# Optimization experiments

Hardware: AMD Instinct MI355X
Metric: run time of the kernel (lower is better)

Reference implementation:

```python
import jax, jax.numpy as jnp
from jax import lax
import numpy as np

H = 64  # hiddenSize
I = 9   # inputSize

def _init_lstm_params(key, in_dim, hidden):
    k = 1.0 / np.sqrt(hidden)
    ks = jax.random.split(key, 4)
    w_ih = jax.random.uniform(ks[0], (4 * hidden, in_dim), minval=-k, maxval=k, dtype=jnp.float32)
    w_hh = jax.random.uniform(ks[1], (4 * hidden, hidden), minval=-k, maxval=k, dtype=jnp.float32)
    b_ih = jax.random.uniform(ks[2], (4 * hidden,), minval=-k, maxval=k, dtype=jnp.float32)
    b_hh = jax.random.uniform(ks[3], (4 * hidden,), minval=-k, maxval=k, dtype=jnp.float32)
    return w_ih, w_hh, b_ih, b_hh

def setup_inputs() -> dict:
    key = jax.random.key(0)
    kx, k0, k1, kl = jax.random.split(key, 4)
    x = jax.random.normal(kx, (4096, 336, I), dtype=jnp.float32)
    w_ih0, w_hh0, b_ih0, b_hh0 = _init_lstm_params(k0, I, H)
    w_ih1, w_hh1, b_ih1, b_hh1 = _init_lstm_params(k1, H, H)
    klw, klb = jax.random.split(kl)
    k = 1.0 / np.sqrt(H)
    w_lin = jax.random.uniform(klw, (1, H), minval=-k, maxval=k, dtype=jnp.float32)
    b_lin = jax.random.uniform(klb, (1,), minval=-k, maxval=k, dtype=jnp.float32)
    return {"x": x, "w_ih0": w_ih0, "w_hh0": w_hh0, "b_ih0": b_ih0, "b_hh0": b_hh0,
            "w_ih1": w_ih1, "w_hh1": w_hh1, "b_ih1": b_ih1, "b_hh1": b_hh1,
            "w_lin": w_lin, "b_lin": b_lin}

def _lstm_layer(x_seq, w_ih, w_hh, b_ih, b_hh):
    # x_seq: [B, T, D] -> hidden sequence [B, T, H]. PyTorch gate order: i, f, g, o.
    B = x_seq.shape[0]
    hidden = w_hh.shape[1]
    # Precompute input contribution for all timesteps in one GEMM.
    pre = jnp.einsum('btd,gd->btg', x_seq, w_ih) + b_ih + b_hh  # [B, T, 4H]
    pre_t = jnp.swapaxes(pre, 0, 1)  # [T, B, 4H]

    def step(carry, p):
        h, c = carry
        gates = p + h @ w_hh.T  # [B, 4H]
        i, f, g, o = jnp.split(gates, 4, axis=-1)
        i = jax.nn.sigmoid(i)
        f = jax.nn.sigmoid(f)
        g = jnp.tanh(g)
        o = jax.nn.sigmoid(o)
        c = f * c + i * g
        h = o * jnp.tanh(c)
        return (h, c), h

    h0 = jnp.zeros((B, hidden), dtype=x_seq.dtype)
    c0 = jnp.zeros((B, hidden), dtype=x_seq.dtype)
    _, hs = lax.scan(step, (h0, c0), pre_t)
    return jnp.swapaxes(hs, 0, 1)  # [B, T, H]

def reference(x, w_ih0, w_hh0, b_ih0, b_hh0, w_ih1, w_hh1, b_ih1, b_hh1, w_lin, b_lin):
    h1 = _lstm_layer(x, w_ih0, w_hh0, b_ih0, b_hh0)     # layer 1 (dropout inactive in eval)
    h2 = _lstm_layer(h1, w_ih1, w_hh1, b_ih1, b_hh1)    # layer 2
    last = h2[:, -1, :]                                  # [B, H]
    out = jax.nn.sigmoid(last @ w_lin.T + b_lin)         # [B, 1]
    return out
```

## Files before the change

### kernel.cpp

```cpp
#include <hip/hip_runtime.h>
#include <hip/hip_bf16.h>
#include <stdint.h>


typedef __attribute__((ext_vector_type(8))) short s16x8;
typedef __attribute__((ext_vector_type(4))) short s16x4;
typedef __attribute__((ext_vector_type(4))) float f32x4;

#define MFMA_BF16 __builtin_amdgcn_mfma_f32_16x16x32_bf16
#define LOG2E     1.4426950408889634f
#define TWO_LOG2E 2.8853900817779268f

__device__ __forceinline__ short f2bf(float f) {
    uint32_t u = __builtin_bit_cast(uint32_t, f);
    u += 0x7fffu + ((u >> 16) & 1u);
    return (short)(u >> 16);
}

__device__ __forceinline__ s16x4 pack_bf16x4(float a, float b, float c, float d) {
    union { uint32_t u[2]; s16x4 s; } r;
    asm("v_cvt_pk_bf16_f32 %0, %1, %2" : "=v"(r.u[0]) : "v"(a), "v"(b));
    asm("v_cvt_pk_bf16_f32 %0, %1, %2" : "=v"(r.u[1]) : "v"(c), "v"(d));
    return r.s;
}

static __device__ __forceinline__ float fexp2(float t){ return __builtin_amdgcn_exp2f(t); }
static __device__ __forceinline__ float frcp (float t){ return __builtin_amdgcn_rcpf(t); }

__device__ __forceinline__ float rcp1p2(float t) {
    return frcp(1.0f + fexp2(t));
}

__device__ __forceinline__ f32x4 nonlin_wide(const f32x4 acc[4], f32x4& cs) {
    float e0[4], e1[4], e2[4], e3[4];
    #pragma unroll
    for (int r = 0; r < 4; ++r) {
        e0[r] = fexp2(acc[0][r]);
        e1[r] = fexp2(acc[1][r]);
        e2[r] = fexp2(acc[2][r]);
        e3[r] = fexp2(acc[3][r]);
    }
    float iv[4], fv[4], gq[4], ov[4];
    #pragma unroll
    for (int r = 0; r < 4; ++r) {
        iv[r] = frcp(1.f + e0[r]);
        fv[r] = frcp(1.f + e1[r]);
        gq[r] = frcp(1.f + e2[r]);
        ov[r] = frcp(1.f + e3[r]);
    }
    float ec[4];
    #pragma unroll
    for (int r = 0; r < 4; ++r) {
        float gvs = fmaf(-2.f * TWO_LOG2E, gq[r], TWO_LOG2E);
        cs[r] = fmaf(fv[r], cs[r], iv[r] * gvs);
        ec[r] = fexp2(cs[r]);
    }
    f32x4 h;
    #pragma unroll
    for (int r = 0; r < 4; ++r) {
        float th = fmaf(-2.f, frcp(1.f + ec[r]), 1.f);
        h[r] = ov[r] * th;
    }
    return h;
}

__global__ __launch_bounds__(512, 1)
void lstm_fused(const float* __restrict__ x,
                const float* __restrict__ w_ih0, const float* __restrict__ w_hh0,
                const float* __restrict__ b_ih0, const float* __restrict__ b_hh0,
                const float* __restrict__ w_ih1, const float* __restrict__ w_hh1,
                const float* __restrict__ b_ih1, const float* __restrict__ b_hh1,
                const float* __restrict__ w_lin, const float* __restrict__ b_lin,
                float* __restrict__ out)
{
    __shared__ __align__(16) short xs[16 * 512];
    __shared__ __align__(16) short h0s[2][16 * 64];
    __shared__ __align__(16) short h1s[16 * 64];
    __shared__ float red[4][16];

    const int tid  = threadIdx.x;
    const int w    = tid >> 6;
    const int role = w >> 2;
    const int wl   = w & 3;
    const int l    = tid & 63;
    const int bcol = l & 15;
    const int q    = l >> 4;
    const int b0   = blockIdx.x * 16;

    for (int i = tid; i < 16 * 512; i += 512) xs[i] = 0;
    for (int i = tid; i < 16 * 64; i += 512) {
        h0s[0][i] = 0; h0s[1][i] = 0; h1s[i] = 0;
    }
    __syncthreads();

    const float scm[4] = { -LOG2E, -LOG2E, TWO_LOG2E, -LOG2E };

    s16x8 aW[4][4];
    f32x4 bias[4];
    #pragma unroll
    for (int m = 0; m < 4; ++m) {
        const int R = m * 64 + wl * 16 + bcol;
        const float sc = scm[m];
        if (role == 0) {
            #pragma unroll
            for (int r = 0; r < 8; ++r) {
                int k = q * 8 + r;
                aW[m][0][r] = (k < 9) ? f2bf(w_ih0[R * 9 + k] * sc) : (short)0;
            }
            #pragma unroll
            for (int kf = 0; kf < 2; ++kf) {
                const float* p = w_hh0 + R * 64 + kf * 32 + q * 8;
                #pragma unroll
                for (int r = 0; r < 8; ++r) aW[m][1 + kf][r] = f2bf(p[r] * sc);
            }
            #pragma unroll
            for (int r = 0; r < 8; ++r) aW[m][3][r] = 0;
            #pragma unroll
            for (int r = 0; r < 4; ++r) {
                int G = m * 64 + wl * 16 + q * 4 + r;
                bias[m][r] = (b_ih0[G] + b_hh0[G]) * sc;
            }
        } else {
            #pragma unroll
            for (int kf = 0; kf < 4; ++kf) {
                int ks = kf * 32 + q * 8;
                const float* p = (ks < 64) ? (w_ih1 + R * 64 + ks)
                                           : (w_hh1 + R * 64 + (ks - 64));
                #pragma unroll
                for (int r = 0; r < 8; ++r) aW[m][kf][r] = f2bf(p[r] * sc);
            }
            #pragma unroll
            for (int r = 0; r < 4; ++r) {
                int G = m * 64 + wl * 16 + q * 4 + r;
                bias[m][r] = (b_ih1[G] + b_hh1[G]) * sc;
            }
        }
    }

    f32x4 cs = {0.f, 0.f, 0.f, 0.f};
    f32x4 hq = {0.f, 0.f, 0.f, 0.f};
    f32x4 accL1[4];
    #pragma unroll
    for (int m = 0; m < 4; ++m) accL1[m] = (f32x4){0.f, 0.f, 0.f, 0.f};

    const int hrd0 = bcol * 64 + (((q    ) ^ (bcol & 7)) << 3);
    const int hrd1 = bcol * 64 + (((4 + q) ^ (bcol & 7)) << 3);
    const int hwr  = bcol * 64 + (((wl * 2 + (q >> 1)) ^ (bcol & 7)) << 3)
                   + ((q & 1) << 2);
    const int xrd  = bcol * 32 + ((q ^ (bcol & 3)) << 3);

    const int    ld_b = (tid & 255) >> 4, ld_t = tid & 15;
    const float* xrow = x + (size_t)(b0 + ld_b) * (336 * 9) + ld_t * 9;
    const int    xs_wr_base = ld_t * 512 + ld_b * 32;
    const int    xswzw = (ld_b & 3) << 3;

    #pragma unroll 1
    for (int i = 0; i <= 337; ++i) {
        if ((i & 15) == 0 && i < 336) {
            if (tid < 256) {
                const float* xp = xrow + (size_t)i * 9;
                #pragma unroll
                for (int d = 0; d < 9; ++d)
                    xs[(xs_wr_base + d) ^ xswzw] = f2bf(xp[d]);
            }
            __syncthreads();
        }

        f32x4 acc0[4];
        s16x8 ba1, bb1;
        if (role == 0) {
            if (i <= 335) {
                s16x8 bx = *(const s16x8*)&xs[(i & 15) * 512 + xrd];
                const short* h0r = h0s[(i & 1) ^ 1];
                s16x8 ba = *(const s16x8*)&h0r[hrd0];
                s16x8 bb = *(const s16x8*)&h0r[hrd1];
                #pragma unroll
                for (int m = 0; m < 4; ++m) acc0[m] = MFMA_BF16(aW[m][0], bx, bias[m], 0, 0, 0);
                #pragma unroll
                for (int m = 0; m < 4; ++m) acc0[m] = MFMA_BF16(aW[m][1], ba, acc0[m], 0, 0, 0);
                #pragma unroll
                for (int m = 0; m < 4; ++m) acc0[m] = MFMA_BF16(aW[m][2], bb, acc0[m], 0, 0, 0);
            }
        } else {
            if (i >= 1 && i <= 336) {
                const short* h0r = h0s[(i & 1) ^ 1];
                ba1 = *(const s16x8*)&h0r[hrd0];
                bb1 = *(const s16x8*)&h0r[hrd1];
            }
            if (i >= 2) {
                __builtin_amdgcn_s_setprio(1);
                hq = nonlin_wide(accL1, cs);
                __builtin_amdgcn_s_setprio(0);
                *(s16x4*)&h1s[hwr] = pack_bf16x4(hq[0], hq[1], hq[2], hq[3]);
            }
        }
        __syncthreads();

        if (role == 0) {
            if (i <= 335) {
                __builtin_amdgcn_s_setprio(1);
                hq = nonlin_wide(acc0, cs);
                __builtin_amdgcn_s_setprio(0);
                short* h0w = h0s[i & 1];
                *(s16x4*)&h0w[hwr] = pack_bf16x4(hq[0], hq[1], hq[2], hq[3]);
            }
        } else {
            if (i >= 1 && i <= 336) {
                s16x8 b1a = *(const s16x8*)&h1s[hrd0];
                s16x8 b1b = *(const s16x8*)&h1s[hrd1];
                #pragma unroll
                for (int m = 0; m < 4; ++m) accL1[m] = MFMA_BF16(aW[m][0], ba1, bias[m], 0, 0, 0);
                #pragma unroll
                for (int m = 0; m < 4; ++m) accL1[m] = MFMA_BF16(aW[m][1], bb1, accL1[m], 0, 0, 0);
                #pragma unroll
                for (int m = 0; m < 4; ++m) accL1[m] = MFMA_BF16(aW[m][2], b1a, accL1[m], 0, 0, 0);
                #pragma unroll
                for (int m = 0; m < 4; ++m) accL1[m] = MFMA_BF16(aW[m][3], b1b, accL1[m], 0, 0, 0);
            }
        }
        __syncthreads();
    }

    if (role == 1) {
        float part = hq[0] * w_lin[wl * 16 + q * 4 + 0]
                   + hq[1] * w_lin[wl * 16 + q * 4 + 1]
                   + hq[2] * w_lin[wl * 16 + q * 4 + 2]
                   + hq[3] * w_lin[wl * 16 + q * 4 + 3];
        part += __shfl_xor(part, 16, 64);
        part += __shfl_xor(part, 32, 64);
        if (q == 0) red[wl][bcol] = part;
    }
    __syncthreads();
    if (tid < 16) {
        float s = red[0][tid] + red[1][tid] + red[2][tid] + red[3][tid] + b_lin[0];
        out[b0 + tid] = rcp1p2(-s * LOG2E);
    }
}

extern "C" void kernel_launch(void* const* d_in, const int* in_sizes, int n_in,
                              void* d_out, int out_size, void* d_ws, size_t ws_size,
                              hipStream_t stream) {
    const float* x     = (const float*)d_in[0];
    const float* w_ih0 = (const float*)d_in[1];
    const float* w_hh0 = (const float*)d_in[2];
    const float* b_ih0 = (const float*)d_in[3];
    const float* b_hh0 = (const float*)d_in[4];
    const float* w_ih1 = (const float*)d_in[5];
    const float* w_hh1 = (const float*)d_in[6];
    const float* b_ih1 = (const float*)d_in[7];
    const float* b_hh1 = (const float*)d_in[8];
    const float* w_lin = (const float*)d_in[9];
    const float* b_lin = (const float*)d_in[10];

    lstm_fused<<<dim3(256), dim3(512), 0, stream>>>(
        x, w_ih0, w_hh0, b_ih0, b_hh0,
        w_ih1, w_hh1, b_ih1, b_hh1,
        w_lin, b_lin, (float*)d_out);
}
```

Measured before the change: 278.1 us.

## Split LSTM gate nonlinearity into two stages across barrier phases

Splits the gate nonlinearity into a first stage (gate sigmoids and the i*g product) and a second stage (cell update and tanh). The first stage now runs right after the MFMAs in the same phase, before the barrier. Only the short cell-state stage stays on the critical path after the barrier, which is meant to shorten the serial recurrence per timestep and balance work between the two layer roles. It keeps extra per-gate registers alive across the barrier and adds a sched_barrier that limits compiler reordering.

```diff
diff --git a/kernel.cpp b/kernel.cpp
--- a/kernel.cpp
+++ b/kernel.cpp
@@ -31,7 +31,8 @@
     return frcp(1.0f + fexp2(t));
 }
 
-__device__ __forceinline__ f32x4 nonlin_wide(const f32x4 acc[4], f32x4& cs) {
+__device__ __forceinline__ void nl_s1(const f32x4 acc[4],
+                                      float fv[4], float ig[4], float ov[4]) {
     float e0[4], e1[4], e2[4], e3[4];
     #pragma unroll
     for (int r = 0; r < 4; ++r) {
@@ -40,26 +41,28 @@
         e2[r] = fexp2(acc[2][r]);
         e3[r] = fexp2(acc[3][r]);
     }
-    float iv[4], fv[4], gq[4], ov[4];
-    #pragma unroll
-    for (int r = 0; r < 4; ++r) {
-        iv[r] = frcp(1.f + e0[r]);
-        fv[r] = frcp(1.f + e1[r]);
-        gq[r] = frcp(1.f + e2[r]);
-        ov[r] = frcp(1.f + e3[r]);
-    }
+    #pragma unroll
+    for (int r = 0; r < 4; ++r) {
+        float iv = frcp(1.f + e0[r]);
+        fv[r]    = frcp(1.f + e1[r]);
+        float gq = frcp(1.f + e2[r]);
+        ov[r]    = frcp(1.f + e3[r]);
+        float gvs = fmaf(-2.f * TWO_LOG2E, gq, TWO_LOG2E);
+        ig[r] = iv * gvs;
+    }
+}
+__device__ __forceinline__ f32x4 nl_s2(const float fv[4], const float ig[4],
+                                       const float ov[4], f32x4& cs) {
     float ec[4];
     #pragma unroll
     for (int r = 0; r < 4; ++r) {
-        float gvs = fmaf(-2.f * TWO_LOG2E, gq[r], TWO_LOG2E);
-        cs[r] = fmaf(fv[r], cs[r], iv[r] * gvs);
+        cs[r] = fmaf(fv[r], cs[r], ig[r]);
         ec[r] = fexp2(cs[r]);
     }
     f32x4 h;
     #pragma unroll
     for (int r = 0; r < 4; ++r) {
-        float th = fmaf(-2.f, frcp(1.f + ec[r]), 1.f);
-        h[r] = ov[r] * th;
+        h[r] = ov[r] * fmaf(-2.f, frcp(1.f + ec[r]), 1.f);
     }
     return h;
 }
@@ -139,9 +142,13 @@
 
     f32x4 cs = {0.f, 0.f, 0.f, 0.f};
     f32x4 hq = {0.f, 0.f, 0.f, 0.f};
-    f32x4 accL1[4];
-    #pragma unroll
-    for (int m = 0; m < 4; ++m) accL1[m] = (f32x4){0.f, 0.f, 0.f, 0.f};
+    float fv0[4], ig0[4], ov0[4];
+    float fv1[4], ig1[4], ov1[4];
+    #pragma unroll
+    for (int k = 0; k < 4; ++k) {
+        fv0[k] = 0.f; ig0[k] = 0.f; ov0[k] = 0.f;
+        fv1[k] = 0.f; ig1[k] = 0.f; ov1[k] = 0.f;
+    }
 
     const int hrd0 = bcol * 64 + (((q    ) ^ (bcol & 7)) << 3);
     const int hrd1 = bcol * 64 + (((4 + q) ^ (bcol & 7)) << 3);
@@ -166,7 +173,6 @@
             __syncthreads();
         }
 
-        f32x4 acc0[4];
         s16x8 ba1, bb1;
         if (role == 0) {
             if (i <= 335) {
@@ -174,12 +180,15 @@
                 const short* h0r = h0s[(i & 1) ^ 1];
                 s16x8 ba = *(const s16x8*)&h0r[hrd0];
                 s16x8 bb = *(const s16x8*)&h0r[hrd1];
+                f32x4 acc0[4];
                 #pragma unroll
                 for (int m = 0; m < 4; ++m) acc0[m] = MFMA_BF16(aW[m][0], bx, bias[m], 0, 0, 0);
                 #pragma unroll
                 for (int m = 0; m < 4; ++m) acc0[m] = MFMA_BF16(aW[m][1], ba, acc0[m], 0, 0, 0);
                 #pragma unroll
                 for (int m = 0; m < 4; ++m) acc0[m] = MFMA_BF16(aW[m][2], bb, acc0[m], 0, 0, 0);
+                nl_s1(acc0, fv0, ig0, ov0);
+                __builtin_amdgcn_sched_barrier(0);
             }
         } else {
             if (i >= 1 && i <= 336) {
@@ -189,7 +198,7 @@
             }
             if (i >= 2) {
                 __builtin_amdgcn_s_setprio(1);
-                hq = nonlin_wide(accL1, cs);
+                hq = nl_s2(fv1, ig1, ov1, cs);
                 __builtin_amdgcn_s_setprio(0);
                 *(s16x4*)&h1s[hwr] = pack_bf16x4(hq[0], hq[1], hq[2], hq[3]);
             }
@@ -199,7 +208,7 @@
         if (role == 0) {
             if (i <= 335) {
                 __builtin_amdgcn_s_setprio(1);
-                hq = nonlin_wide(acc0, cs);
+                hq = nl_s2(fv0, ig0, ov0, cs);
                 __builtin_amdgcn_s_setprio(0);
                 short* h0w = h0s[i & 1];
                 *(s16x4*)&h0w[hwr] = pack_bf16x4(hq[0], hq[1], hq[2], hq[3]);
@@ -208,6 +217,7 @@
             if (i >= 1 && i <= 336) {
                 s16x8 b1a = *(const s16x8*)&h1s[hrd0];
                 s16x8 b1b = *(const s16x8*)&h1s[hrd1];
+                f32x4 accL1[4];
                 #pragma unroll
                 for (int m = 0; m < 4; ++m) accL1[m] = MFMA_BF16(aW[m][0], ba1, bias[m], 0, 0, 0);
                 #pragma unroll
@@ -216,6 +226,8 @@
                 for (int m = 0; m < 4; ++m) accL1[m] = MFMA_BF16(aW[m][2], b1a, accL1[m], 0, 0, 0);
                 #pragma unroll
                 for (int m = 0; m < 4; ++m) accL1[m] = MFMA_BF16(aW[m][3], b1b, accL1[m], 0, 0, 0);
+                nl_s1(accL1, fv1, ig1, ov1);
+                __builtin_amdgcn_sched_barrier(0);
             }
         }
         __syncthreads();
```

Result: slower. 289.1 us (+4.0%).
